# Kernel tuning notes

Hardware: AMD Instinct MI355X
Metric: run time of the kernel (lower is better)

## Reference

```python
import jax, jax.numpy as jnp
import numpy as np
from jax import lax

VOCAB, VEC, HID, L, BATCH, OPT, K = 50000, 256, 256, 256, 8, 4, 2
H2, H8 = 2 * HID, 8 * HID


def _gru_dir(x, wih, whh, bih, bhh, reverse):
    # x: [B, L, D]; PyTorch GRU cell math.
    B = x.shape[0]
    H = whh.shape[1]
    def step(h, xt):
        gi = xt @ wih.T + bih            # [B, 3H]
        gh = h @ whh.T + bhh             # [B, 3H]
        ir, iz, inn = jnp.split(gi, 3, axis=-1)
        hr, hz, hn = jnp.split(gh, 3, axis=-1)
        r = jax.nn.sigmoid(ir + hr)
        z = jax.nn.sigmoid(iz + hz)
        n = jnp.tanh(inn + r * hn)
        hnew = (1.0 - z) * n + z * h
        return hnew, hnew
    h0 = jnp.zeros((B, H), x.dtype)
    _, ys = lax.scan(step, h0, jnp.swapaxes(x, 0, 1), reverse=reverse)
    return jnp.swapaxes(ys, 0, 1)        # [B, L, H]


def _bigru(x, wih, whh, bih, bhh):
    f = _gru_dir(x, wih[0], whh[0], bih[0], bhh[0], False)
    b = _gru_dir(x, wih[1], whh[1], bih[1], bhh[1], True)
    return jnp.concatenate([f, b], axis=-1)


def _bidaf(c, q, w, b):
    # s[b,i,j] = w_c.c_i + w_q.q_j + sum_d c_id*q_jd*w_cq_d + (b_c+b_q+b_cq)
    s = (c @ w[0])[:, :, None] + (q @ w[1])[:, None, :] \
        + jnp.einsum('bcd,bqd->bcq', c * w[2], q) + (b[0] + b[1] + b[2])
    a = jax.nn.softmax(s, axis=2)
    c2q = jnp.einsum('bcq,bqd->bcd', a, q)
    bb = jax.nn.softmax(jnp.max(s, axis=2), axis=1)        # [B, c_len]
    q2c = jnp.einsum('bc,bcd->bd', bb, c)[:, None, :]       # [B, 1, D]
    return jnp.concatenate([c, c2q, c * c2q, c * q2c], axis=-1)


def setup_inputs() -> dict:
    key = jax.random.key(0)
    ks = jax.random.split(key, 20)
    s = 0.05
    return {
        'question': jax.random.randint(ks[0], (BATCH, OPT, L), 0, VOCAB),
        'article': jax.random.randint(ks[1], (BATCH, OPT * K, L), 0, VOCAB),
        'emb': jax.random.normal(ks[2], (VOCAB, VEC), jnp.float32),
        'g1_wih': jax.random.normal(ks[3], (2, 3 * HID, VEC), jnp.float32) * s,
        'g1_whh': jax.random.normal(ks[4], (2, 3 * HID, HID), jnp.float32) * s,
        'g1_bih': jax.random.normal(ks[5], (2, 3 * HID), jnp.float32) * s,
        'g1_bhh': jax.random.normal(ks[6], (2, 3 * HID), jnp.float32) * s,
        'g2_wih': jax.random.normal(ks[7], (2, 3 * HID, H8), jnp.float32) * s,
        'g2_whh': jax.random.normal(ks[8], (2, 3 * HID, HID), jnp.float32) * s,
        'g2_bih': jax.random.normal(ks[9], (2, 3 * HID), jnp.float32) * s,
        'g2_bhh': jax.random.normal(ks[10], (2, 3 * HID), jnp.float32) * s,
        'b1_w': jax.random.normal(ks[11], (3, H2), jnp.float32) * s,
        'b1_b': jax.random.normal(ks[12], (3,), jnp.float32) * s,
        'b2_w': jax.random.normal(ks[13], (3, H2), jnp.float32) * s,
        'b2_b': jax.random.normal(ks[14], (3,), jnp.float32) * s,
        'rank_w': jax.random.normal(ks[15], (H8 * L,), jnp.float32) * 0.002,
        'rank_b': jax.random.normal(ks[16], (1,), jnp.float32) * s,
        'k': K,
        'option': OPT,
    }


def reference(question, article, emb, g1_wih, g1_whh, g1_bih, g1_bhh,
              g2_wih, g2_whh, g2_bih, g2_bhh, b1_w, b1_b, b2_w, b2_b,
              rank_w, rank_b, k, option):
    batch, _, max_len = question.shape
    # question.repeat(1,1,k).view(B*opt*k, L)
    q_ids = jnp.tile(question, (1, 1, k)).reshape(batch * option * k, max_len)
    a_ids = article.reshape(batch * option * k, max_len)
    qx = emb[q_ids]                                  # [Beff, L, VEC]
    ax = emb[a_ids]
    qh = _bigru(qx, g1_wih, g1_whh, g1_bih, g1_bhh)  # shared encoder, [Beff, L, 2H]
    ah = _bigru(ax, g1_wih, g1_whh, g1_bih, g1_bhh)
    att = jax.nn.relu(_bidaf(qh, ah, b1_w, b1_b))    # [Beff, L, 8H]
    ax2 = _bigru(att, g2_wih, g2_whh, g2_bih, g2_bhh)  # [Beff, L, 2H]
    ax2 = jax.nn.relu(_bidaf(ax2, ax2, b2_w, b2_b))    # [Beff, L, 8H]
    s = att + ax2
    # rank_method == 'max': max over k copies, then linear
    y = s.reshape(batch * option, k, -1)
    y = jnp.max(y, axis=1)                           # [B*opt, L*8H]
    y = y @ rank_w + rank_b[0]                       # [B*opt]
    return y.reshape(batch, option)
```

## Files before the change

kernel.cpp:

```cpp
#include <hip/hip_runtime.h>
#include <math.h>

#define LSEQ 256
#define HID 256
#define H2 512
#define H3 768
#define H8 2048

typedef __attribute__((ext_vector_type(8))) short short8;
typedef __attribute__((ext_vector_type(4))) float floatx4;

__device__ __forceinline__ unsigned short f2bf(float f) {
    unsigned int u = __float_as_uint(f);
    u = (u + 0x7FFFu + ((u >> 16) & 1u)) >> 16;
    return (unsigned short)u;
}
__device__ __forceinline__ float bf2f(unsigned short h) {
    return __uint_as_float(((unsigned int)h) << 16);
}
__device__ __forceinline__ float fsig(float x) {
    return __builtin_amdgcn_rcpf(1.f + __expf(-x));
}
__device__ __forceinline__ float ftanh(float x) {
    return __builtin_fmaf(2.f, __builtin_amdgcn_rcpf(1.f + __expf(-2.f * x)), -1.f);
}
__device__ __forceinline__ void bfsplit(float x, unsigned short& hi, unsigned short& lo) {
    hi = f2bf(x);
    lo = f2bf(x - bf2f(hi));
}
__device__ __forceinline__ void gload_lds16(const void* g, void* l) {
    __builtin_amdgcn_global_load_lds(
        (const __attribute__((address_space(1))) unsigned int*)g,
        (__attribute__((address_space(3))) unsigned int*)l, 16, 0, 0);
}

__global__ void embed_kernel(const int* __restrict__ question,
                             const int* __restrict__ article,
                             const float* __restrict__ emb,
                             unsigned short* __restrict__ xemb) {
    int gid = blockIdx.x * 256 + threadIdx.x;
    int d = gid & 255;
    int rl = gid >> 8;
    int l = rl & 255;
    int stream = rl >> 8;
    int id;
    if (stream < 64) {
        int b = stream >> 3, o = (stream & 7) >> 1;
        id = question[(b * 4 + o) * 256 + l];
    } else {
        id = article[(stream - 64) * 256 + l];
    }
    xemb[(size_t)gid] = f2bf(emb[(size_t)id * 256 + d]);
}

__global__ void pack_bf8(const float* __restrict__ src, unsigned short* __restrict__ dst, int n8) {
    int i = blockIdx.x * 256 + threadIdx.x;
    if (i >= n8) return;
    float4 a = ((const float4*)src)[2 * i];
    float4 b = ((const float4*)src)[2 * i + 1];
    uint4 o;
    o.x = (unsigned int)f2bf(a.x) | ((unsigned int)f2bf(a.y) << 16);
    o.y = (unsigned int)f2bf(a.z) | ((unsigned int)f2bf(a.w) << 16);
    o.z = (unsigned int)f2bf(b.x) | ((unsigned int)f2bf(b.y) << 16);
    o.w = (unsigned int)f2bf(b.z) | ((unsigned int)f2bf(b.w) << 16);
    ((uint4*)dst)[i] = o;
}

__global__ void pack_weights(const float* __restrict__ g1whh, const float* __restrict__ g1wih,
                             const float* __restrict__ g2whh, const float* __restrict__ g2wih,
                             unsigned short* __restrict__ wpk1, unsigned short* __restrict__ wih1,
                             unsigned short* __restrict__ wpk2, unsigned short* __restrict__ wih2) {
    int i = blockIdx.x * 256 + threadIdx.x;
    const float* src; unsigned short* dst; int j;
    if (i < 49152)       { src = g1whh; dst = wpk1; j = i; }
    else if (i < 98304)  { src = g1wih; dst = wih1; j = i - 49152; }
    else if (i < 147456) { src = g2whh; dst = wpk2; j = i - 98304; }
    else if (i < 540672) { src = g2wih; dst = wih2; j = i - 147456; }
    else return;
    float4 a = ((const float4*)src)[2 * j];
    float4 b = ((const float4*)src)[2 * j + 1];
    uint4 o;
    o.x = (unsigned int)f2bf(a.x) | ((unsigned int)f2bf(a.y) << 16);
    o.y = (unsigned int)f2bf(a.z) | ((unsigned int)f2bf(a.w) << 16);
    o.z = (unsigned int)f2bf(b.x) | ((unsigned int)f2bf(b.y) << 16);
    o.w = (unsigned int)f2bf(b.z) | ((unsigned int)f2bf(b.w) << 16);
    ((uint4*)dst)[j] = o;
}

__global__ __launch_bounds__(256)
void gemm_2dir(const unsigned short* __restrict__ A, const unsigned short* __restrict__ B,
               const float* __restrict__ bias, unsigned short* __restrict__ C0,
               unsigned short* __restrict__ C1, int mbase, int K) {
    __shared__ __align__(16) unsigned short At[128][32];
    __shared__ __align__(16) unsigned short Bt[128][32];
    int tid = threadIdx.x;
    int m0 = blockIdx.x * 128, n0 = blockIdx.y * 128;
    int l = tid & 63, w = tid >> 6;
    int wm = (w & 1) * 64, wn = (w >> 1) * 64;
    int lr = l & 15, kq = l >> 4;
    int subrow = l >> 2;
    int swc = (l & 3) ^ (subrow & 3);
    const unsigned short* gA0 = A + (size_t)(m0 + w * 32 + subrow) * K + swc * 8;
    const unsigned short* gA1 = A + (size_t)(m0 + w * 32 + 16 + subrow) * K + swc * 8;
    const unsigned short* gB0 = B + (size_t)(n0 + w * 32 + subrow) * K + swc * 8;
    const unsigned short* gB1 = B + (size_t)(n0 + w * 32 + 16 + subrow) * K + swc * 8;
    unsigned short* lA0 = &At[w * 32][0];
    unsigned short* lA1 = &At[w * 32 + 16][0];
    unsigned short* lB0 = &Bt[w * 32][0];
    unsigned short* lB1 = &Bt[w * 32 + 16][0];
    int rchunk = (kq ^ (lr & 3)) * 8;
    floatx4 acc[4][4];
#pragma unroll
    for (int i = 0; i < 4; i++)
#pragma unroll
        for (int j = 0; j < 4; j++) acc[i][j] = (floatx4){0.f, 0.f, 0.f, 0.f};
    for (int k0 = 0; k0 < K; k0 += 32) {
        __syncthreads();
        gload_lds16(gA0 + k0, lA0);
        gload_lds16(gA1 + k0, lA1);
        gload_lds16(gB0 + k0, lB0);
        gload_lds16(gB1 + k0, lB1);
        __syncthreads();
        short8 af[4], bf[4];
#pragma unroll
        for (int i = 0; i < 4; i++) {
            af[i] = *(const short8*)&At[wm + i * 16 + lr][rchunk];
            bf[i] = *(const short8*)&Bt[wn + i * 16 + lr][rchunk];
        }
#pragma unroll
        for (int i = 0; i < 4; i++)
#pragma unroll
            for (int j = 0; j < 4; j++)
                acc[i][j] = __builtin_amdgcn_mfma_f32_16x16x32_bf16(af[i], bf[j], acc[i][j], 0, 0, 0);
    }
    int quad = l >> 4;
#pragma unroll
    for (int i = 0; i < 4; i++) {
#pragma unroll
        for (int j = 0; j < 4; j++) {
            int n = n0 + wn + j * 16 + lr;
            float bs = bias[n];
            unsigned short* dst = (n < 768) ? C0 : C1;
            int nn = (n < 768) ? n : n - 768;
#pragma unroll
            for (int r = 0; r < 4; r++) {
                int m = mbase + m0 + wm + i * 16 + quad * 4 + r;
                dst[(size_t)m * 768 + nn] = f2bf(acc[i][j][r] + bs);
            }
        }
    }
}

__global__ __launch_bounds__(512, 2)
void gru_scan_rreg(const unsigned short* __restrict__ gi_f,
                   const unsigned short* __restrict__ gi_b,
                   const unsigned short* __restrict__ whh_bf,
                   const float* __restrict__ bhh,
                   float* __restrict__ out) {
    int blk = blockIdx.x;
    int d = blk & 1, s = blk >> 1;
    const unsigned short* gi_blk = (d ? gi_b : gi_f) + (size_t)s * LSEQ * H3;
    const unsigned short* wb = whh_bf + (size_t)d * H3 * HID;

    __shared__ __align__(16) unsigned short h_pack[2][256];

    int tid = threadIdx.x;
    int lane = tid & 63, wave = tid >> 6;
    int lr = lane & 15, kq = lane >> 4;

    short8 bq[6][8];
#pragma unroll
    for (int nt = 0; nt < 6; nt++) {
        int row = (nt >> 1) * 256 + wave * 32 + (nt & 1) * 16 + lr;
        const unsigned short* wp = wb + (size_t)row * HID + kq * 8;
#pragma unroll
        for (int kt = 0; kt < 8; kt++)
            bq[nt][kt] = *(const short8*)(wp + kt * 32);
    }

    int hh0 = wave * 32 + lr, hh1 = hh0 + 16;
    float br0 = bhh[d * H3 + hh0],       br1 = bhh[d * H3 + hh1];
    float bz0 = bhh[d * H3 + 256 + hh0], bz1 = bhh[d * H3 + 256 + hh1];
    float bn0 = bhh[d * H3 + 512 + hh0], bn1 = bhh[d * H3 + 512 + hh1];

    int t0 = d ? (LSEQ - 1) : 0;
    int tstep = d ? -1 : 1;

    if (tid < 128) ((unsigned int*)h_pack[0])[tid] = 0;
    float hold0 = 0.f, hold1 = 0.f;

    unsigned short gr0, gz0, gn0, gr1, gz1, gn1;
    {
        const unsigned short* gp = gi_blk + (size_t)t0 * H3;
        gr0 = gp[hh0]; gz0 = gp[256 + hh0]; gn0 = gp[512 + hh0];
        gr1 = gp[hh1]; gz1 = gp[256 + hh1]; gn1 = gp[512 + hh1];
    }
    __syncthreads();

    int cur = 0, t = t0;
    for (int step = 0; step < LSEQ; ++step) {
        unsigned short nr0 = 0, nz0 = 0, nn0 = 0, nr1 = 0, nz1 = 0, nn1 = 0;
        if (step + 1 < LSEQ) {
            const unsigned short* gp = gi_blk + (size_t)(t + tstep) * H3;
            nr0 = gp[hh0]; nz0 = gp[256 + hh0]; nn0 = gp[512 + hh0];
            nr1 = gp[hh1]; nz1 = gp[256 + hh1]; nn1 = gp[512 + hh1];
        }
        floatx4 acc[6];
#pragma unroll
        for (int nt = 0; nt < 6; nt++) acc[nt] = (floatx4){0.f, 0.f, 0.f, 0.f};
#pragma unroll
        for (int kt = 0; kt < 8; kt++) {
            short8 av = *(const short8*)&h_pack[cur][kt * 32 + kq * 8];
#pragma unroll
            for (int nt = 0; nt < 6; nt++)
                acc[nt] = __builtin_amdgcn_mfma_f32_16x16x32_bf16(av, bq[nt][kt], acc[nt], 0, 0, 0);
        }
        float rg0 = fsig(bf2f(gr0) + acc[0][0] + br0);
        float rg1 = fsig(bf2f(gr1) + acc[1][0] + br1);
        float zg0 = fsig(bf2f(gz0) + acc[2][0] + bz0);
        float zg1 = fsig(bf2f(gz1) + acc[3][0] + bz1);
        float ng0 = ftanh(bf2f(gn0) + rg0 * (acc[4][0] + bn0));
        float ng1 = ftanh(bf2f(gn1) + rg1 * (acc[5][0] + bn1));
        float h0 = (1.f - zg0) * ng0 + zg0 * hold0;
        float h1 = (1.f - zg1) * ng1 + zg1 * hold1;
        hold0 = h0; hold1 = h1;
        int nxt = cur ^ 1;
        if (kq == 0) {
            h_pack[nxt][hh0] = f2bf(h0);
            h_pack[nxt][hh1] = f2bf(h1);
            float* op = out + ((size_t)s * LSEQ + t) * H2 + d * HID;
            op[hh0] = h0;
            op[hh1] = h1;
        }
        gr0 = nr0; gz0 = nz0; gn0 = nn0;
        gr1 = nr1; gz1 = nz1; gn1 = nn1;
        __syncthreads();
        cur = nxt; t += tstep;
    }
}

__global__ void cwqw_kernel(const float* __restrict__ c, const float* __restrict__ q,
                            const float* __restrict__ w,
                            float* __restrict__ cw, float* __restrict__ qw) {
    int row = blockIdx.x;
    int lane = threadIdx.x;
    const float* src; const float* wv; float* dst; int r;
    if (row < 16384) { src = c; wv = w; dst = cw; r = row; }
    else { src = q; wv = w + 512; dst = qw; r = row - 16384; }
    const float* p = src + (size_t)r * H2;
    float acc = 0.f;
    for (int j = lane; j < H2; j += 64) acc += p[j] * wv[j];
    for (int off = 32; off; off >>= 1) acc += __shfl_down(acc, off);
    if (lane == 0) dst[r] = acc;
}

__global__ __launch_bounds__(256)
void smat_mfma(const float* __restrict__ c, const float* __restrict__ q,
               const float* __restrict__ w2, const float* __restrict__ bvec,
               const float* __restrict__ cw, const float* __restrict__ qw,
               float* __restrict__ smat) {
    __shared__ __align__(16) unsigned short Ah[128][40];
    __shared__ __align__(16) unsigned short Al[128][40];
    __shared__ __align__(16) unsigned short Bh[128][40];
    __shared__ __align__(16) unsigned short Bl[128][40];
    int b = blockIdx.z;
    int m0 = blockIdx.x * 128, n0 = blockIdx.y * 128;
    int tid = threadIdx.x;
    int l = tid & 63, w = tid >> 6;
    int wm = (w & 1) * 64, wn = (w >> 1) * 64;
    int lr = l & 15, koff = (l >> 4) * 8;
    int srow = tid >> 1, scol = (tid & 1) * 16;
    floatx4 acc[4][4];
#pragma unroll
    for (int i = 0; i < 4; i++)
#pragma unroll
        for (int j = 0; j < 4; j++) acc[i][j] = (floatx4){0.f, 0.f, 0.f, 0.f};
    const float* ap0 = c + (size_t)(b * 256 + m0 + srow) * H2 + scol;
    const float* bp0 = q + (size_t)(b * 256 + n0 + srow) * H2 + scol;
    for (int k0 = 0; k0 < H2; k0 += 32) {
        float av[16], bv[16], wv[16];
        *(float4*)&av[0]  = *(const float4*)(ap0 + k0);
        *(float4*)&av[4]  = *(const float4*)(ap0 + k0 + 4);
        *(float4*)&av[8]  = *(const float4*)(ap0 + k0 + 8);
        *(float4*)&av[12] = *(const float4*)(ap0 + k0 + 12);
        *(float4*)&bv[0]  = *(const float4*)(bp0 + k0);
        *(float4*)&bv[4]  = *(const float4*)(bp0 + k0 + 4);
        *(float4*)&bv[8]  = *(const float4*)(bp0 + k0 + 8);
        *(float4*)&bv[12] = *(const float4*)(bp0 + k0 + 12);
        *(float4*)&wv[0]  = *(const float4*)(w2 + k0 + scol);
        *(float4*)&wv[4]  = *(const float4*)(w2 + k0 + scol + 4);
        *(float4*)&wv[8]  = *(const float4*)(w2 + k0 + scol + 8);
        *(float4*)&wv[12] = *(const float4*)(w2 + k0 + scol + 12);
        unsigned int ahw[8], alw[8], bhw[8], blw[8];
#pragma unroll
        for (int j = 0; j < 8; j++) {
            float p0 = av[2 * j] * wv[2 * j], p1 = av[2 * j + 1] * wv[2 * j + 1];
            unsigned short h0, s0, h1, s1;
            bfsplit(p0, h0, s0); bfsplit(p1, h1, s1);
            ahw[j] = (unsigned int)h0 | ((unsigned int)h1 << 16);
            alw[j] = (unsigned int)s0 | ((unsigned int)s1 << 16);
            unsigned short g0, t0, g1, t1;
            bfsplit(bv[2 * j], g0, t0); bfsplit(bv[2 * j + 1], g1, t1);
            bhw[j] = (unsigned int)g0 | ((unsigned int)g1 << 16);
            blw[j] = (unsigned int)t0 | ((unsigned int)t1 << 16);
        }
        __syncthreads();
        *(uint4*)&Ah[srow][scol]     = *(uint4*)&ahw[0];
        *(uint4*)&Ah[srow][scol + 8] = *(uint4*)&ahw[4];
        *(uint4*)&Al[srow][scol]     = *(uint4*)&alw[0];
        *(uint4*)&Al[srow][scol + 8] = *(uint4*)&alw[4];
        *(uint4*)&Bh[srow][scol]     = *(uint4*)&bhw[0];
        *(uint4*)&Bh[srow][scol + 8] = *(uint4*)&bhw[4];
        *(uint4*)&Bl[srow][scol]     = *(uint4*)&blw[0];
        *(uint4*)&Bl[srow][scol + 8] = *(uint4*)&blw[4];
        __syncthreads();
        short8 afh[4], afl[4], bfh[4], bfl[4];
#pragma unroll
        for (int i = 0; i < 4; i++) {
            afh[i] = *(const short8*)&Ah[wm + i * 16 + lr][koff];
            afl[i] = *(const short8*)&Al[wm + i * 16 + lr][koff];
            bfh[i] = *(const short8*)&Bh[wn + i * 16 + lr][koff];
            bfl[i] = *(const short8*)&Bl[wn + i * 16 + lr][koff];
        }
#pragma unroll
        for (int i = 0; i < 4; i++)
#pragma unroll
            for (int j = 0; j < 4; j++) {
                acc[i][j] = __builtin_amdgcn_mfma_f32_16x16x32_bf16(afl[i], bfh[j], acc[i][j], 0, 0, 0);
                acc[i][j] = __builtin_amdgcn_mfma_f32_16x16x32_bf16(afh[i], bfl[j], acc[i][j], 0, 0, 0);
                acc[i][j] = __builtin_amdgcn_mfma_f32_16x16x32_bf16(afh[i], bfh[j], acc[i][j], 0, 0, 0);
            }
    }
    float bsum = bvec[0] + bvec[1] + bvec[2];
    int quad = l >> 4;
#pragma unroll
    for (int i = 0; i < 4; i++) {
#pragma unroll
        for (int j = 0; j < 4; j++) {
            int n = n0 + wn + j * 16 + lr;
            float qwv = qw[b * 256 + n] + bsum;
#pragma unroll
            for (int r = 0; r < 4; r++) {
                int m = m0 + wm + i * 16 + quad * 4 + r;
                smat[((size_t)(b * 256 + m)) * 256 + n] = acc[i][j][r] + cw[b * 256 + m] + qwv;
            }
        }
    }
}

__global__ void softmax_kernel(float* __restrict__ smat, float* __restrict__ rowmax) {
    int row = blockIdx.x;
    int lane = threadIdx.x;
    float* p = smat + (size_t)row * LSEQ;
    float v[4];
    float mx = -1e30f;
#pragma unroll
    for (int j = 0; j < 4; j++) { v[j] = p[lane + j * 64]; mx = fmaxf(mx, v[j]); }
    for (int off = 32; off; off >>= 1) mx = fmaxf(mx, __shfl_down(mx, off));
    mx = __shfl(mx, 0);
    float sum = 0.f;
#pragma unroll
    for (int j = 0; j < 4; j++) { v[j] = __expf(v[j] - mx); sum += v[j]; }
    for (int off = 32; off; off >>= 1) sum += __shfl_down(sum, off);
    sum = __shfl(sum, 0);
    float inv = 1.f / sum;
#pragma unroll
    for (int j = 0; j < 4; j++) p[lane + j * 64] = v[j] * inv;
    if (lane == 0) rowmax[row] = mx;
}

__global__ void bb_kernel(const float* __restrict__ rowmax, float* __restrict__ bb) {
    int b = blockIdx.x; int t = threadIdx.x;
    __shared__ float red[256];
    float v = rowmax[b * LSEQ + t];
    red[t] = v; __syncthreads();
    for (int s = 128; s; s >>= 1) { if (t < s) red[t] = fmaxf(red[t], red[t + s]); __syncthreads(); }
    float mx = red[0]; __syncthreads();
    float e = __expf(v - mx);
    red[t] = e; __syncthreads();
    for (int s = 128; s; s >>= 1) { if (t < s) red[t] += red[t + s]; __syncthreads(); }
    bb[b * LSEQ + t] = e / red[0];
}

__global__ void q2c_kernel(const float* __restrict__ bb, const float* __restrict__ c,
                           float* __restrict__ q2c) {
    int b = blockIdx.x;
    int d = blockIdx.y * 128 + threadIdx.x;
    const float* cb = c + (size_t)b * LSEQ * H2 + d;
    const float* bbp = bb + b * LSEQ;
    float a0 = 0.f, a1 = 0.f, a2 = 0.f, a3 = 0.f;
    for (int i = 0; i < LSEQ; i += 4) {
        a0 += bbp[i]     * cb[(size_t)i * H2];
        a1 += bbp[i + 1] * cb[(size_t)(i + 1) * H2];
        a2 += bbp[i + 2] * cb[(size_t)(i + 2) * H2];
        a3 += bbp[i + 3] * cb[(size_t)(i + 3) * H2];
    }
    q2c[b * H2 + d] = (a0 + a1) + (a2 + a3);
}

__global__ __launch_bounds__(256)
void c2q_fix_mfma(const float* __restrict__ amat, const float* __restrict__ q,
                  const float* __restrict__ c, const float* __restrict__ q2c,
                  float* __restrict__ att, int add) {
    __shared__ __align__(16) unsigned short Ah[128][40];
    __shared__ __align__(16) unsigned short Al[128][40];
    __shared__ __align__(16) unsigned short Bh[128][40];
    __shared__ __align__(16) unsigned short Bl[128][40];
    int b = blockIdx.z;
    int m0 = blockIdx.x * 128, n0 = blockIdx.y * 128;
    int tid = threadIdx.x;
    int l = tid & 63, w = tid >> 6;
    int wm = (w & 1) * 64, wn = (w >> 1) * 64;
    int lr = l & 15, koff = (l >> 4) * 8;
    int srow = tid >> 1, scol = (tid & 1) * 16;
    int bn = tid & 127, bkh = tid >> 7;
    floatx4 acc[4][4];
#pragma unroll
    for (int i = 0; i < 4; i++)
#pragma unroll
        for (int j = 0; j < 4; j++) acc[i][j] = (floatx4){0.f, 0.f, 0.f, 0.f};
    for (int k0 = 0; k0 < LSEQ; k0 += 32) {
        float av[16];
        const float* ap = amat + (size_t)(b * 256 + m0 + srow) * 256 + k0 + scol;
        *(float4*)&av[0]  = *(const float4*)(ap);
        *(float4*)&av[4]  = *(const float4*)(ap + 4);
        *(float4*)&av[8]  = *(const float4*)(ap + 8);
        *(float4*)&av[12] = *(const float4*)(ap + 12);
        float qv[16];
        const float* qp = q + (size_t)(b * 256 + k0 + bkh * 16) * H2 + n0 + bn;
#pragma unroll
        for (int j = 0; j < 16; j++) qv[j] = qp[(size_t)j * H2];
        unsigned int ahw[8], alw[8], bhw[8], blw[8];
#pragma unroll
        for (int j = 0; j < 8; j++) {
            unsigned short h0, s0, h1, s1;
            bfsplit(av[2 * j], h0, s0); bfsplit(av[2 * j + 1], h1, s1);
            ahw[j] = (unsigned int)h0 | ((unsigned int)h1 << 16);
            alw[j] = (unsigned int)s0 | ((unsigned int)s1 << 16);
            unsigned short g0, t0, g1, t1;
            bfsplit(qv[2 * j], g0, t0); bfsplit(qv[2 * j + 1], g1, t1);
            bhw[j] = (unsigned int)g0 | ((unsigned int)g1 << 16);
            blw[j] = (unsigned int)t0 | ((unsigned int)t1 << 16);
        }
        __syncthreads();
        *(uint4*)&Ah[srow][scol]         = *(uint4*)&ahw[0];
        *(uint4*)&Ah[srow][scol + 8]     = *(uint4*)&ahw[4];
        *(uint4*)&Al[srow][scol]         = *(uint4*)&alw[0];
        *(uint4*)&Al[srow][scol + 8]     = *(uint4*)&alw[4];
        *(uint4*)&Bh[bn][bkh * 16]       = *(uint4*)&bhw[0];
        *(uint4*)&Bh[bn][bkh * 16 + 8]   = *(uint4*)&bhw[4];
        *(uint4*)&Bl[bn][bkh * 16]       = *(uint4*)&blw[0];
        *(uint4*)&Bl[bn][bkh * 16 + 8]   = *(uint4*)&blw[4];
        __syncthreads();
        short8 afh[4], afl[4], bfh[4], bfl[4];
#pragma unroll
        for (int i = 0; i < 4; i++) {
            afh[i] = *(const short8*)&Ah[wm + i * 16 + lr][koff];
            afl[i] = *(const short8*)&Al[wm + i * 16 + lr][koff];
            bfh[i] = *(const short8*)&Bh[wn + i * 16 + lr][koff];
            bfl[i] = *(const short8*)&Bl[wn + i * 16 + lr][koff];
        }
#pragma unroll
        for (int i = 0; i < 4; i++)
#pragma unroll
            for (int j = 0; j < 4; j++) {
                acc[i][j] = __builtin_amdgcn_mfma_f32_16x16x32_bf16(afl[i], bfh[j], acc[i][j], 0, 0, 0);
                acc[i][j] = __builtin_amdgcn_mfma_f32_16x16x32_bf16(afh[i], bfl[j], acc[i][j], 0, 0, 0);
                acc[i][j] = __builtin_amdgcn_mfma_f32_16x16x32_bf16(afh[i], bfh[j], acc[i][j], 0, 0, 0);
            }
    }
    int quad = l >> 4;
#pragma unroll
    for (int i = 0; i < 4; i++) {
#pragma unroll
        for (int j = 0; j < 4; j++) {
            int n = n0 + wn + j * 16 + lr;
            float q2cv = q2c[b * H2 + n];
#pragma unroll
            for (int r = 0; r < 4; r++) {
                int m = m0 + wm + i * 16 + quad * 4 + r;
                size_t row = (size_t)b * 256 + m;
                float a = acc[i][j][r];
                float cv = c[row * H2 + n];
                float v0 = fmaxf(cv, 0.f);
                float v1 = fmaxf(a, 0.f);
                float v2 = fmaxf(cv * a, 0.f);
                float v3 = fmaxf(cv * q2cv, 0.f);
                float* p0 = att + row * H8 + n;
                float* p1 = p0 + 512;
                float* p2 = p0 + 1024;
                float* p3 = p0 + 1536;
                if (add) { *p0 += v0; *p1 += v1; *p2 += v2; *p3 += v3; }
                else     { *p0 = v0;  *p1 = v1;  *p2 = v2;  *p3 = v3; }
            }
        }
    }
}

__global__ void reduce1_kernel(const float* __restrict__ s, const float* __restrict__ rw,
                               float* __restrict__ part) {
    int bo = blockIdx.x;
    int p = blockIdx.y;
    int t = threadIdx.x;
    const float* s0 = s + (size_t)(2 * bo) * 524288;
    const float* s1 = s0 + 524288;
    size_t base = (size_t)p * 65536;
    float acc = 0.f;
    for (int j = t; j < 65536; j += 256) {
        size_t m = base + j;
        acc += rw[m] * fmaxf(s0[m], s1[m]);
    }
    __shared__ float red[256];
    red[t] = acc; __syncthreads();
    for (int ss = 128; ss; ss >>= 1) { if (t < ss) red[t] += red[t + ss]; __syncthreads(); }
    if (t == 0) part[bo * 8 + p] = red[0];
}

__global__ void reduce2_kernel(const float* __restrict__ part, const float* __restrict__ rb,
                               float* __restrict__ out) {
    int t = threadIdx.x;
    float a = rb[0];
    for (int p = 0; p < 8; p++) a += part[t * 8 + p];
    out[t] = a;
}

extern "C" void kernel_launch(void* const* d_in, const int* in_sizes, int n_in,
                              void* d_out, int out_size, void* d_ws, size_t ws_size,
                              hipStream_t stream) {
    const int* question = (const int*)d_in[0];
    const int* article  = (const int*)d_in[1];
    const float* emb    = (const float*)d_in[2];
    const float* g1_wih = (const float*)d_in[3];
    const float* g1_whh = (const float*)d_in[4];
    const float* g1_bih = (const float*)d_in[5];
    const float* g1_bhh = (const float*)d_in[6];
    const float* g2_wih = (const float*)d_in[7];
    const float* g2_whh = (const float*)d_in[8];
    const float* g2_bih = (const float*)d_in[9];
    const float* g2_bhh = (const float*)d_in[10];
    const float* b1_w   = (const float*)d_in[11];
    const float* b1_b   = (const float*)d_in[12];
    const float* b2_w   = (const float*)d_in[13];
    const float* b2_b   = (const float*)d_in[14];
    const float* rank_w = (const float*)d_in[15];
    const float* rank_b = (const float*)d_in[16];
    float* ws = (float*)d_ws;
    float* out = (float*)d_out;

    unsigned short* WPK1  = (unsigned short*)(ws);
    unsigned short* WIH1B = (unsigned short*)(ws + 196608);
    unsigned short* WPK2  = (unsigned short*)(ws + 393216);
    unsigned short* WIH2B = (unsigned short*)(ws + 589824);
    float* CW   = ws + 2162688;
    float* QW   = ws + 2179072;
    float* RM   = ws + 2195456;
    float* BBv  = ws + 2211840;
    float* Q2C  = ws + 2228224;
    float* PART = ws + 2260992;
    unsigned short* XEMBB = (unsigned short*)(ws + 2293760);
    float*          SMAT  = ws + 2293760;
    unsigned short* GI2B  = (unsigned short*)(ws + 2293760);
    float*          HBUF  = ws + 6488064;
    unsigned short* ATTBH = (unsigned short*)(ws + 14876672);
    float*          AX2   = ws + 14876672;
    float*          ATT   = ws + 25165824;
    unsigned short* GI1B  = (unsigned short*)(ws + 25165824);

    embed_kernel<<<32768, 256, 0, stream>>>(question, article, emb, XEMBB);
    pack_weights<<<2112, 256, 0, stream>>>(g1_whh, g1_wih, g2_whh, g2_wih,
                                           WPK1, WIH1B, WPK2, WIH2B);

    gemm_2dir<<<dim3(256, 12), 256, 0, stream>>>(
        XEMBB, WIH1B, g1_bih, GI1B, GI1B + (size_t)25165824, 0, 256);
    gru_scan_rreg<<<256, 512, 0, stream>>>(GI1B, GI1B + (size_t)25165824, WPK1, g1_bhh, HBUF);

    float* QH = HBUF;
    float* AH = HBUF + (size_t)64 * 256 * 512;

    {
        cwqw_kernel<<<32768, 64, 0, stream>>>(QH, AH, b1_w, CW, QW);
        smat_mfma<<<dim3(2, 2, 64), 256, 0, stream>>>(QH, AH, b1_w + 1024, b1_b, CW, QW, SMAT);
        softmax_kernel<<<16384, 64, 0, stream>>>(SMAT, RM);
        bb_kernel<<<64, 256, 0, stream>>>(RM, BBv);
        q2c_kernel<<<dim3(64, 4), 128, 0, stream>>>(BBv, QH, Q2C);
        c2q_fix_mfma<<<dim3(2, 4, 64), 256, 0, stream>>>(SMAT, AH, QH, Q2C, ATT, 0);
    }

    for (int half = 0; half < 2; half++) {
        pack_bf8<<<8192, 256, 0, stream>>>(ATT + (size_t)half * 16777216, ATTBH, 2097152);
        gemm_2dir<<<dim3(64, 12), 256, 0, stream>>>(
            ATTBH, WIH2B, g2_bih, GI2B, GI2B + (size_t)12582912, half * 8192, 2048);
    }
    gru_scan_rreg<<<128, 512, 0, stream>>>(GI2B, GI2B + (size_t)12582912, WPK2, g2_bhh, AX2);

    {
        cwqw_kernel<<<32768, 64, 0, stream>>>(AX2, AX2, b2_w, CW, QW);
        smat_mfma<<<dim3(2, 2, 64), 256, 0, stream>>>(AX2, AX2, b2_w + 1024, b2_b, CW, QW, SMAT);
        softmax_kernel<<<16384, 64, 0, stream>>>(SMAT, RM);
        bb_kernel<<<64, 256, 0, stream>>>(RM, BBv);
        q2c_kernel<<<dim3(64, 4), 128, 0, stream>>>(BBv, AX2, Q2C);
        c2q_fix_mfma<<<dim3(2, 4, 64), 256, 0, stream>>>(SMAT, AX2, AX2, Q2C, ATT, 1);
    }

    reduce1_kernel<<<dim3(32, 8), 256, 0, stream>>>(ATT, rank_w, PART);
    reduce2_kernel<<<1, 32, 0, stream>>>(PART, rank_b, out);
}
```

Baseline: 1.322 ms.

## Store attention output as bf16 and fold cw/qw dot products into smat

```diff
diff --git a/kernel.cpp b/kernel.cpp
--- a/kernel.cpp
+++ b/kernel.cpp
@@ -51,19 +51,6 @@
         id = article[(stream - 64) * 256 + l];
     }
     xemb[(size_t)gid] = f2bf(emb[(size_t)id * 256 + d]);
-}
-
-__global__ void pack_bf8(const float* __restrict__ src, unsigned short* __restrict__ dst, int n8) {
-    int i = blockIdx.x * 256 + threadIdx.x;
-    if (i >= n8) return;
-    float4 a = ((const float4*)src)[2 * i];
-    float4 b = ((const float4*)src)[2 * i + 1];
-    uint4 o;
-    o.x = (unsigned int)f2bf(a.x) | ((unsigned int)f2bf(a.y) << 16);
-    o.y = (unsigned int)f2bf(a.z) | ((unsigned int)f2bf(a.w) << 16);
-    o.z = (unsigned int)f2bf(b.x) | ((unsigned int)f2bf(b.y) << 16);
-    o.w = (unsigned int)f2bf(b.z) | ((unsigned int)f2bf(b.w) << 16);
-    ((uint4*)dst)[i] = o;
 }
 
 __global__ void pack_weights(const float* __restrict__ g1whh, const float* __restrict__ g1wih,
@@ -239,30 +226,17 @@
     }
 }
 
-__global__ void cwqw_kernel(const float* __restrict__ c, const float* __restrict__ q,
-                            const float* __restrict__ w,
-                            float* __restrict__ cw, float* __restrict__ qw) {
-    int row = blockIdx.x;
-    int lane = threadIdx.x;
-    const float* src; const float* wv; float* dst; int r;
-    if (row < 16384) { src = c; wv = w; dst = cw; r = row; }
-    else { src = q; wv = w + 512; dst = qw; r = row - 16384; }
-    const float* p = src + (size_t)r * H2;
-    float acc = 0.f;
-    for (int j = lane; j < H2; j += 64) acc += p[j] * wv[j];
-    for (int off = 32; off; off >>= 1) acc += __shfl_down(acc, off);
-    if (lane == 0) dst[r] = acc;
-}
-
 __global__ __launch_bounds__(256)
 void smat_mfma(const float* __restrict__ c, const float* __restrict__ q,
-               const float* __restrict__ w2, const float* __restrict__ bvec,
-               const float* __restrict__ cw, const float* __restrict__ qw,
+               const float* __restrict__ w1, const float* __restrict__ bvec,
                float* __restrict__ smat) {
     __shared__ __align__(16) unsigned short Ah[128][40];
     __shared__ __align__(16) unsigned short Al[128][40];
     __shared__ __align__(16) unsigned short Bh[128][40];
     __shared__ __align__(16) unsigned short Bl[128][40];
+    __shared__ float cwl[128];
+    __shared__ float qwl[128];
+    const float* w2 = w1 + 1024;
     int b = blockIdx.z;
     int m0 = blockIdx.x * 128, n0 = blockIdx.y * 128;
     int tid = threadIdx.x;
@@ -277,8 +251,9 @@
         for (int j = 0; j < 4; j++) acc[i][j] = (floatx4){0.f, 0.f, 0.f, 0.f};
     const float* ap0 = c + (size_t)(b * 256 + m0 + srow) * H2 + scol;
     const float* bp0 = q + (size_t)(b * 256 + n0 + srow) * H2 + scol;
+    float pcw = 0.f, pqw = 0.f;
     for (int k0 = 0; k0 < H2; k0 += 32) {
-        float av[16], bv[16], wv[16];
+        float av[16], bv[16], wv[16], wc[16], wq[16];
         *(float4*)&av[0]  = *(const float4*)(ap0 + k0);
         *(float4*)&av[4]  = *(const float4*)(ap0 + k0 + 4);
         *(float4*)&av[8]  = *(const float4*)(ap0 + k0 + 8);
@@ -291,6 +266,16 @@
         *(float4*)&wv[4]  = *(const float4*)(w2 + k0 + scol + 4);
         *(float4*)&wv[8]  = *(const float4*)(w2 + k0 + scol + 8);
         *(float4*)&wv[12] = *(const float4*)(w2 + k0 + scol + 12);
+        *(float4*)&wc[0]  = *(const float4*)(w1 + k0 + scol);
+        *(float4*)&wc[4]  = *(const float4*)(w1 + k0 + scol + 4);
+        *(float4*)&wc[8]  = *(const float4*)(w1 + k0 + scol + 8);
+        *(float4*)&wc[12] = *(const float4*)(w1 + k0 + scol + 12);
+        *(float4*)&wq[0]  = *(const float4*)(w1 + 512 + k0 + scol);
+        *(float4*)&wq[4]  = *(const float4*)(w1 + 512 + k0 + scol + 4);
+        *(float4*)&wq[8]  = *(const float4*)(w1 + 512 + k0 + scol + 8);
+        *(float4*)&wq[12] = *(const float4*)(w1 + 512 + k0 + scol + 12);
+#pragma unroll
+        for (int j = 0; j < 16; j++) { pcw += av[j] * wc[j]; pqw += bv[j] * wq[j]; }
         unsigned int ahw[8], alw[8], bhw[8], blw[8];
 #pragma unroll
         for (int j = 0; j < 8; j++) {
@@ -331,6 +316,10 @@
                 acc[i][j] = __builtin_amdgcn_mfma_f32_16x16x32_bf16(afh[i], bfh[j], acc[i][j], 0, 0, 0);
             }
     }
+    pcw += __shfl_xor(pcw, 1);
+    pqw += __shfl_xor(pqw, 1);
+    if ((tid & 1) == 0) { cwl[srow] = pcw; qwl[srow] = pqw; }
+    __syncthreads();
     float bsum = bvec[0] + bvec[1] + bvec[2];
     int quad = l >> 4;
 #pragma unroll
@@ -338,11 +327,12 @@
 #pragma unroll
         for (int j = 0; j < 4; j++) {
             int n = n0 + wn + j * 16 + lr;
-            float qwv = qw[b * 256 + n] + bsum;
+            float qwv = qwl[wn + j * 16 + lr] + bsum;
 #pragma unroll
             for (int r = 0; r < 4; r++) {
                 int m = m0 + wm + i * 16 + quad * 4 + r;
-                smat[((size_t)(b * 256 + m)) * 256 + n] = acc[i][j][r] + cw[b * 256 + m] + qwv;
+                smat[((size_t)(b * 256 + m)) * 256 + n] =
+                    acc[i][j][r] + cwl[wm + i * 16 + quad * 4 + r] + qwv;
             }
         }
     }
@@ -401,7 +391,7 @@
 __global__ __launch_bounds__(256)
 void c2q_fix_mfma(const float* __restrict__ amat, const float* __restrict__ q,
                   const float* __restrict__ c, const float* __restrict__ q2c,
-                  float* __restrict__ att, int add) {
+                  unsigned short* __restrict__ att, int add) {
     __shared__ __align__(16) unsigned short Ah[128][40];
     __shared__ __align__(16) unsigned short Al[128][40];
     __shared__ __align__(16) unsigned short Bh[128][40];
@@ -486,29 +476,36 @@
                 float v1 = fmaxf(a, 0.f);
                 float v2 = fmaxf(cv * a, 0.f);
                 float v3 = fmaxf(cv * q2cv, 0.f);
-                float* p0 = att + row * H8 + n;
-                float* p1 = p0 + 512;
-                float* p2 = p0 + 1024;
-                float* p3 = p0 + 1536;
-                if (add) { *p0 += v0; *p1 += v1; *p2 += v2; *p3 += v3; }
-                else     { *p0 = v0;  *p1 = v1;  *p2 = v2;  *p3 = v3; }
+                unsigned short* p0 = att + row * H8 + n;
+                if (add) {
+                    p0[0]    = f2bf(bf2f(p0[0])    + v0);
+                    p0[512]  = f2bf(bf2f(p0[512])  + v1);
+                    p0[1024] = f2bf(bf2f(p0[1024]) + v2);
+                    p0[1536] = f2bf(bf2f(p0[1536]) + v3);
+                } else {
+                    p0[0] = f2bf(v0); p0[512] = f2bf(v1);
+                    p0[1024] = f2bf(v2); p0[1536] = f2bf(v3);
+                }
             }
         }
     }
 }
 
-__global__ void reduce1_kernel(const float* __restrict__ s, const float* __restrict__ rw,
+__global__ void reduce1_kernel(const unsigned short* __restrict__ s, const float* __restrict__ rw,
                                float* __restrict__ part) {
     int bo = blockIdx.x;
     int p = blockIdx.y;
     int t = threadIdx.x;
-    const float* s0 = s + (size_t)(2 * bo) * 524288;
-    const float* s1 = s0 + 524288;
-    size_t base = (size_t)p * 65536;
+    const unsigned int* s0 = (const unsigned int*)(s + (size_t)(2 * bo) * 524288 + (size_t)p * 65536);
+    const unsigned int* s1 = (const unsigned int*)(s + (size_t)(2 * bo) * 524288 + 524288 + (size_t)p * 65536);
+    const float* rwp = rw + (size_t)p * 65536;
     float acc = 0.f;
-    for (int j = t; j < 65536; j += 256) {
-        size_t m = base + j;
-        acc += rw[m] * fmaxf(s0[m], s1[m]);
+    for (int j = t; j < 32768; j += 256) {
+        unsigned int a = s0[j], b = s1[j];
+        float2 rv = *(const float2*)(rwp + 2 * j);
+        float x0 = fmaxf(__uint_as_float(a << 16), __uint_as_float(b << 16));
+        float x1 = fmaxf(__uint_as_float(a & 0xFFFF0000u), __uint_as_float(b & 0xFFFF0000u));
+        acc += rv.x * x0 + rv.y * x1;
     }
     __shared__ float red[256];
     red[t] = acc; __syncthreads();
@@ -551,8 +548,6 @@
     unsigned short* WIH1B = (unsigned short*)(ws + 196608);
     unsigned short* WPK2  = (unsigned short*)(ws + 393216);
     unsigned short* WIH2B = (unsigned short*)(ws + 589824);
-    float* CW   = ws + 2162688;
-    float* QW   = ws + 2179072;
     float* RM   = ws + 2195456;
     float* BBv  = ws + 2211840;
     float* Q2C  = ws + 2228224;
@@ -561,9 +556,8 @@
     float*          SMAT  = ws + 2293760;
     unsigned short* GI2B  = (unsigned short*)(ws + 2293760);
     float*          HBUF  = ws + 6488064;
-    unsigned short* ATTBH = (unsigned short*)(ws + 14876672);
     float*          AX2   = ws + 14876672;
-    float*          ATT   = ws + 25165824;
+    unsigned short* ATTB  = (unsigned short*)(ws + 25165824);
     unsigned short* GI1B  = (unsigned short*)(ws + 25165824);
 
     embed_kernel<<<32768, 256, 0, stream>>>(question, article, emb, XEMBB);
@@ -578,30 +572,25 @@
     float* AH = HBUF + (size_t)64 * 256 * 512;
 
     {
-        cwqw_kernel<<<32768, 64, 0, stream>>>(QH, AH, b1_w, CW, QW);
-        smat_mfma<<<dim3(2, 2, 64), 256, 0, stream>>>(QH, AH, b1_w + 1024, b1_b, CW, QW, SMAT);
+        smat_mfma<<<dim3(2, 2, 64), 256, 0, stream>>>(QH, AH, b1_w, b1_b, SMAT);
         softmax_kernel<<<16384, 64, 0, stream>>>(SMAT, RM);
         bb_kernel<<<64, 256, 0, stream>>>(RM, BBv);
         q2c_kernel<<<dim3(64, 4), 128, 0, stream>>>(BBv, QH, Q2C);
-        c2q_fix_mfma<<<dim3(2, 4, 64), 256, 0, stream>>>(SMAT, AH, QH, Q2C, ATT, 0);
-    }
-
-    for (int half = 0; half < 2; half++) {
-        pack_bf8<<<8192, 256, 0, stream>>>(ATT + (size_t)half * 16777216, ATTBH, 2097152);
-        gemm_2dir<<<dim3(64, 12), 256, 0, stream>>>(
-            ATTBH, WIH2B, g2_bih, GI2B, GI2B + (size_t)12582912, half * 8192, 2048);
-    }
+        c2q_fix_mfma<<<dim3(2, 4, 64), 256, 0, stream>>>(SMAT, AH, QH, Q2C, ATTB, 0);
+    }
+
+    gemm_2dir<<<dim3(128, 12), 256, 0, stream>>>(
+        ATTB, WIH2B, g2_bih, GI2B, GI2B + (size_t)12582912, 0, 2048);
     gru_scan_rreg<<<128, 512, 0, stream>>>(GI2B, GI2B + (size_t)12582912, WPK2, g2_bhh, AX2);
 
     {
-        cwqw_kernel<<<32768, 64, 0, stream>>>(AX2, AX2, b2_w, CW, QW);
-        smat_mfma<<<dim3(2, 2, 64), 256, 0, stream>>>(AX2, AX2, b2_w + 1024, b2_b, CW, QW, SMAT);
+        smat_mfma<<<dim3(2, 2, 64), 256, 0, stream>>>(AX2, AX2, b2_w, b2_b, SMAT);
         softmax_kernel<<<16384, 64, 0, stream>>>(SMAT, RM);
         bb_kernel<<<64, 256, 0, stream>>>(RM, BBv);
         q2c_kernel<<<dim3(64, 4), 128, 0, stream>>>(BBv, AX2, Q2C);
-        c2q_fix_mfma<<<dim3(2, 4, 64), 256, 0, stream>>>(SMAT, AX2, AX2, Q2C, ATT, 1);
-    }
-
-    reduce1_kernel<<<dim3(32, 8), 256, 0, stream>>>(ATT, rank_w, PART);
+        c2q_fix_mfma<<<dim3(2, 4, 64), 256, 0, stream>>>(SMAT, AX2, AX2, Q2C, ATTB, 1);
+    }
+
+    reduce1_kernel<<<dim3(32, 8), 256, 0, stream>>>(ATTB, rank_w, PART);
     reduce2_kernel<<<1, 32, 0, stream>>>(PART, rank_b, out);
 }
```

Measured after the change: 1.180 ms. 10.7% less time.
